# Kernel tuning notes

Measured on AMD Instinct MI355X. Metric: run time of the kernel, lower is better.

Reference implementation:

```python
import jax, jax.numpy as jnp
import numpy as np

N = 50000      # total nodes (batched graphs)
E = 800000     # edges per hop-set
B = 128        # number of graphs in batch
F_IN = 1024    # num_features_pro
D = 128        # hidden*16, heads=1


def setup_inputs() -> dict:
    key = jax.random.key(0)
    ks = jax.random.split(key, 32)
    s = 0.05
    def ei(k):
        return jax.random.randint(k, (2, E), 0, N, dtype=jnp.int32)
    inp = {
        'pro1_x': jax.random.normal(ks[0], (N, F_IN), jnp.float32),
        'pro1_ei1': ei(ks[1]), 'pro1_ei2': ei(ks[2]), 'pro1_ei3': ei(ks[3]),
        'pro1_batch': jnp.sort(jax.random.randint(ks[4], (N,), 0, B, dtype=jnp.int32)),
        'pro2_x': jax.random.normal(ks[5], (N, F_IN), jnp.float32),
        'pro2_ei1': ei(ks[6]), 'pro2_ei2': ei(ks[7]), 'pro2_ei3': ei(ks[8]),
        'pro2_batch': jnp.sort(jax.random.randint(ks[9], (N,), 0, B, dtype=jnp.int32)),
        # GATConv params (pro1_conv1 / pro2_conv1), shared across hop sets per branch
        'W1': jax.random.normal(ks[10], (F_IN, D), jnp.float32) * s,
        'a1_src': jax.random.normal(ks[11], (D,), jnp.float32) * s,
        'a1_dst': jax.random.normal(ks[12], (D,), jnp.float32) * s,
        'b1': jnp.zeros((D,), jnp.float32),
        'p1fc_W': jax.random.normal(ks[13], (D, D), jnp.float32) * s,
        'p1fc_b': jnp.zeros((D,), jnp.float32),
        'W2': jax.random.normal(ks[14], (F_IN, D), jnp.float32) * s,
        'a2_src': jax.random.normal(ks[15], (D,), jnp.float32) * s,
        'a2_dst': jax.random.normal(ks[16], (D,), jnp.float32) * s,
        'b2': jnp.zeros((D,), jnp.float32),
        'p2fc_W': jax.random.normal(ks[17], (D, D), jnp.float32) * s,
        'p2fc_b': jnp.zeros((D,), jnp.float32),
        'fc1_W': jax.random.normal(ks[18], (2 * D, 256), jnp.float32) * s,
        'fc1_b': jnp.zeros((256,), jnp.float32),
        'fc2_W': jax.random.normal(ks[19], (256, 64), jnp.float32) * s,
        'fc2_b': jnp.zeros((64,), jnp.float32),
        'out_W': jax.random.normal(ks[20], (64, 1), jnp.float32) * s,
        'out_b': jnp.zeros((1,), jnp.float32),
    }
    return inp


def _gat(x, ei, W, a_src, a_dst, b):
    # PyG GATConv, heads=1, add_self_loops=True, dropout off (eval)
    n = x.shape[0]
    h = x @ W                                   # [N, D]
    loops = jnp.arange(n, dtype=ei.dtype)
    src = jnp.concatenate([ei[0], loops])
    dst = jnp.concatenate([ei[1], loops])
    al_s = h @ a_src                            # [N]
    al_d = h @ a_dst
    e = jax.nn.leaky_relu(al_s[src] + al_d[dst], 0.2)   # per-edge logits
    m = jax.ops.segment_max(e, dst, num_segments=n)
    ex = jnp.exp(e - m[dst])
    denom = jax.ops.segment_sum(ex, dst, num_segments=n)
    alpha = ex / denom[dst]
    out = jax.ops.segment_sum(alpha[:, None] * h[src], dst, num_segments=n)
    return out + b


def _lrelu(v):
    return jax.nn.leaky_relu(v, 0.01)  # nn.LeakyReLU default slope


def _branch(x, e1, e2, e3, batch, W, a_s, a_d, b, fcW, fcb):
    h = _lrelu(_gat(x, e1, W, a_s, a_d, b))
    h = h + _lrelu(_gat(x, e2, W, a_s, a_d, b))
    h = h + _lrelu(_gat(x, e3, W, a_s, a_d, b))  # num_hops>=2 branch taken
    counts = jax.ops.segment_sum(jnp.ones((x.shape[0],), x.dtype), batch, num_segments=B)
    pooled = jax.ops.segment_sum(h, batch, num_segments=B) / jnp.maximum(counts, 1.0)[:, None]
    return _lrelu(pooled @ fcW + fcb)


def reference(pro1_x, pro1_ei1, pro1_ei2, pro1_ei3, pro1_batch,
              pro2_x, pro2_ei1, pro2_ei2, pro2_ei3, pro2_batch,
              W1, a1_src, a1_dst, b1, p1fc_W, p1fc_b,
              W2, a2_src, a2_dst, b2, p2fc_W, p2fc_b,
              fc1_W, fc1_b, fc2_W, fc2_b, out_W, out_b):
    x1 = _branch(pro1_x, pro1_ei1, pro1_ei2, pro1_ei3, pro1_batch, W1, a1_src, a1_dst, b1, p1fc_W, p1fc_b)
    x2 = _branch(pro2_x, pro2_ei1, pro2_ei2, pro2_ei3, pro2_batch, W2, a2_src, a2_dst, b2, p2fc_W, p2fc_b)
    xc = jnp.concatenate([x1, x2], axis=1)      # [B, 256]
    xc = _lrelu(xc @ fc1_W + fc1_b)
    xc = _lrelu(xc @ fc2_W + fc2_b)
    return jax.nn.sigmoid(xc @ out_W + out_b)   # [B, 1]
```

## Files before the change

kernel.cpp:

```cpp
#include <hip/hip_runtime.h>
#include <hip/hip_bf16.h>
#include <math.h>

#define N_NODES 50000
#define N_EDGES 800000
#define N_GRAPH 128
#define F_IN    1024
#define D_HID   128
#define NT3     (3*N_NODES)
#define LOG2E   1.44269504f

#define NPB_SH  9
#define NPB     512
#define NB      ((NT3 + NPB - 1) / NPB)
#define CAP     10240
#define EPB     4096
#define NBIN_PB ((3*N_EDGES + EPB - 1) / EPB)

typedef __bf16 bf16x8 __attribute__((ext_vector_type(8)));
typedef float  f32x4  __attribute__((ext_vector_type(4)));
typedef float  f32x2  __attribute__((ext_vector_type(2)));

__device__ __forceinline__ float lrelu01(float x){ return x > 0.f ? x : 0.01f*x; }
__device__ __forceinline__ float lrelu02(float x){ return x > 0.f ? x : 0.2f*x; }
__device__ __forceinline__ ushort f2bf(float v){
    __hip_bfloat16 hb = __float2bfloat16(v);
    return *reinterpret_cast<ushort*>(&hb);
}
__device__ __forceinline__ unsigned char f2fp8(float v){
    return (unsigned char)(__builtin_amdgcn_cvt_pk_fp8_f32(v, v, 0, false) & 0xFF);
}
__device__ __forceinline__ void fma8f8(uint2 u, float w, float* acc){
    f32x2 a = __builtin_amdgcn_cvt_pk_f32_fp8(u.x, false);
    f32x2 b = __builtin_amdgcn_cvt_pk_f32_fp8(u.x, true);
    f32x2 c = __builtin_amdgcn_cvt_pk_f32_fp8(u.y, false);
    f32x2 d = __builtin_amdgcn_cvt_pk_f32_fp8(u.y, true);
    acc[0] += w*a[0]; acc[1] += w*a[1]; acc[2] += w*b[0]; acc[3] += w*b[1];
    acc[4] += w*c[0]; acc[5] += w*c[1]; acc[6] += w*d[0]; acc[7] += w*d[1];
}

__global__ void k_prep(const float* __restrict__ W0, const float* __restrict__ W1,
                       ushort* __restrict__ Wt, int* __restrict__ gcur){
    int b = blockIdx.x, t = threadIdx.x;
    if (b < 1024){
        int idx = b*256 + t;
        int br  = idx >> 17;
        int r   = idx & 131071;
        int n = r >> 10, k = r & 1023;
        const float* W = br ? W1 : W0;
        Wt[idx] = f2bf(W[k*D_HID + n]);
    } else {
        for (int i=t; i<2*NB; i+=256) gcur[i] = 0;
    }
}

#define BM  64
#define BK  64
#define LDP 72

__global__ __launch_bounds__(256) void k_gemm(const float* __restrict__ X0, const float* __restrict__ X1,
                                              const ushort* __restrict__ Wt,
                                              const float* __restrict__ as0, const float* __restrict__ ad0,
                                              const float* __restrict__ as1, const float* __restrict__ ad1,
                                              unsigned char* __restrict__ H8,
                                              float* __restrict__ als, float* __restrict__ ald){
    __shared__ ushort As[BM*LDP];
    __shared__ ushort Bs[D_HID*LDP];
    __shared__ float alp[4][2][64];
    int br = blockIdx.y;
    const float*  X   = br ? X1 : X0;
    const float*  asr = br ? as1 : as0;
    const float*  adr = br ? ad1 : ad0;
    const ushort* Wtb = Wt + (size_t)br*D_HID*F_IN;
    unsigned char* Hbb = H8 + (size_t)br*N_NODES*D_HID;

    int tid  = threadIdx.x;
    int m0   = blockIdx.x * BM;
    int lane = tid & 63;
    int wave = tid >> 6;
    int l15 = lane & 15, l4 = lane >> 4;
    int wcol = wave * 32;

    float4 pa[4];
    uint4  pb[4];

    auto loadA = [&](int kt){
        #pragma unroll
        for (int i=0;i<4;i++){
            int q = tid + i*256; int row = q >> 4; int kq = (q & 15) << 2;
            int gr = m0 + row;
            pa[i] = (gr < N_NODES) ? *reinterpret_cast<const float4*>(X + (size_t)gr*F_IN + kt + kq)
                                   : make_float4(0.f,0.f,0.f,0.f);
        }
    };
    auto loadB = [&](int kt){
        #pragma unroll
        for (int i=0;i<4;i++){
            int q = tid + i*256; int row = q >> 3; int ck = q & 7;
            pb[i] = *reinterpret_cast<const uint4*>(Wtb + row*F_IN + kt + ck*8);
        }
    };
    auto stage = [&](){
        #pragma unroll
        for (int i=0;i<4;i++){
            int q = tid + i*256; int row = q >> 4; int kq = (q & 15) << 2;
            ushort4 b; b.x=f2bf(pa[i].x); b.y=f2bf(pa[i].y); b.z=f2bf(pa[i].z); b.w=f2bf(pa[i].w);
            *reinterpret_cast<ushort4*>(&As[row*LDP + kq]) = b;
        }
        #pragma unroll
        for (int i=0;i<4;i++){
            int q = tid + i*256; int row = q >> 3; int ck = q & 7;
            *reinterpret_cast<uint2*>(&Bs[row*LDP + ck*8])     = make_uint2(pb[i].x, pb[i].y);
            *reinterpret_cast<uint2*>(&Bs[row*LDP + ck*8 + 4]) = make_uint2(pb[i].z, pb[i].w);
        }
    };

    f32x4 acc[4][2];
    #pragma unroll
    for (int i=0;i<4;i++) for (int j=0;j<2;j++) acc[i][j] = (f32x4){0.f,0.f,0.f,0.f};

    loadA(0); loadB(0);
    for (int kt = 0; kt < F_IN; kt += BK) {
        stage();
        __syncthreads();
        if (kt + BK < F_IN){ loadA(kt+BK); loadB(kt+BK); }
        #pragma unroll
        for (int kk = 0; kk < BK; kk += 32) {
            bf16x8 af[4], bfr[2];
            #pragma unroll
            for (int mi=0;mi<4;mi++)
                af[mi] = *reinterpret_cast<const bf16x8*>(&As[(mi*16+l15)*LDP + kk + l4*8]);
            #pragma unroll
            for (int ni=0;ni<2;ni++)
                bfr[ni] = *reinterpret_cast<const bf16x8*>(&Bs[(wcol+ni*16+l15)*LDP + kk + l4*8]);
            #pragma unroll
            for (int mi=0;mi<4;mi++)
                #pragma unroll
                for (int ni=0;ni<2;ni++)
                    acc[mi][ni] = __builtin_amdgcn_mfma_f32_16x16x32_bf16(af[mi], bfr[ni], acc[mi][ni], 0,0,0);
        }
        __syncthreads();
    }

    float asv[2], adv[2];
    #pragma unroll
    for (int ni=0;ni<2;ni++){
        int c = wcol + ni*16 + l15;
        asv[ni] = asr[c]; adv[ni] = adr[c];
    }
    #pragma unroll
    for (int mi=0;mi<4;mi++){
        #pragma unroll
        for (int jj=0;jj<4;jj++){
            int rrel = mi*16 + l4*4 + jj;
            int r = m0 + rrel;
            float ps = 0.f, pd = 0.f;
            #pragma unroll
            for (int ni=0;ni<2;ni++){
                float v = acc[mi][ni][jj];
                ps += v*asv[ni]; pd += v*adv[ni];
                if (r < N_NODES){
                    int c = wcol + ni*16 + l15;
                    Hbb[(size_t)r*D_HID + c] = f2fp8(v);
                }
            }
            #pragma unroll
            for (int o=1;o<16;o<<=1){ ps += __shfl_xor(ps,o); pd += __shfl_xor(pd,o); }
            if (l15 == 0){ alp[wave][0][rrel] = ps; alp[wave][1][rrel] = pd; }
        }
    }
    __syncthreads();
    if (tid < 64){
        int r = m0 + tid;
        if (r < N_NODES){
            float s_ = alp[0][0][tid]+alp[1][0][tid]+alp[2][0][tid]+alp[3][0][tid];
            float d_ = alp[0][1][tid]+alp[1][1][tid]+alp[2][1][tid]+alp[3][1][tid];
            als[br*N_NODES + r] = s_;
            ald[br*N_NODES + r] = d_;
        }
    }
}

__global__ __launch_bounds__(256) void k_bin(const int* __restrict__ e10, const int* __restrict__ e20,
                                             const int* __restrict__ e30,
                                             const int* __restrict__ e11, const int* __restrict__ e21,
                                             const int* __restrict__ e31,
                                             int* __restrict__ gcur, uint* __restrict__ pairs){
    __shared__ int hist[NB];
    __shared__ int start[NB];
    int blk = blockIdx.x;
    int br    = blk / NBIN_PB;
    int chunk = blk - br*NBIN_PB;
    int tid = threadIdx.x;
    for (int b=tid; b<NB; b+=256) hist[b]=0;
    __syncthreads();
    long base = (long)chunk * EPB;
    int  myb[16]; uint mypk[16];
    #pragma unroll
    for (int i=0;i<16;i++){
        long idx = base + i*256 + tid;
        int b = -1; uint pk = 0;
        if (idx < 3L*N_EDGES){
            int hop = (idx >= 2L*N_EDGES) ? 2 : (idx >= (long)N_EDGES) ? 1 : 0;
            int e   = (int)(idx - (long)hop*N_EDGES);
            const int* ei = (br==0) ? ((hop==0)?e10:(hop==1)?e20:e30)
                                    : ((hop==0)?e11:(hop==1)?e21:e31);
            int src = ei[e];
            int vd  = hop*N_NODES + ei[N_EDGES + e];
            b   = vd >> NPB_SH;
            pk  = (uint)src | ((uint)(vd & (NPB-1)) << 16);
            atomicAdd(&hist[b], 1);
        }
        myb[i]=b; mypk[i]=pk;
    }
    __syncthreads();
    for (int b=tid; b<NB; b+=256){
        int h = hist[b];
        start[b] = (h>0) ? atomicAdd(&gcur[br*NB + b], h) : 0;
    }
    __syncthreads();
    for (int b=tid; b<NB; b+=256) hist[b] = start[b];
    __syncthreads();
    #pragma unroll
    for (int i=0;i<16;i++){
        int b = myb[i];
        if (b >= 0){
            int pos = atomicAdd(&hist[b], 1);
            if (pos < CAP) pairs[((size_t)(br*NB + b))*CAP + pos] = mypk[i];
        }
    }
}

__global__ __launch_bounds__(256) void k_localcsr(const int* __restrict__ gcur,
                                                  const uint* __restrict__ pairs,
                                                  int* __restrict__ offs3, int* __restrict__ esrc){
    __shared__ int sc[512];
    __shared__ int deg[NPB];
    __shared__ int cur[NPB];
    __shared__ int ss[256];
    int gb = blockIdx.x;
    int br = gb / NB, bb = gb - br*NB;
    int t = threadIdx.x;
    sc[t]     = (t < NB)       ? min(gcur[br*NB + t], CAP) : 0;
    sc[t+256] = (t+256 < NB)   ? min(gcur[br*NB + t+256], CAP) : 0;
    __syncthreads();
    for (int o=1;o<512;o<<=1){
        int v0 = (t>=o)     ? sc[t-o]     : 0;
        int v1 = (t+256>=o) ? sc[t+256-o] : 0;
        __syncthreads();
        sc[t] += v0; sc[t+256] += v1;
        __syncthreads();
    }
    int base = (bb==0) ? 0 : sc[bb-1];
    int cnt  = sc[bb] - base;
    int* offsb = offs3 + (size_t)br*(NT3+1);
    if (bb == NB-1 && t == 0) offsb[NT3] = sc[NB-1];

    deg[t]=0; deg[t+256]=0;
    __syncthreads();
    const uint* pbuf = pairs + ((size_t)(br*NB + bb))*CAP;
    for (int i=t; i<cnt; i+=256) atomicAdd(&deg[pbuf[i] >> 16], 1);
    __syncthreads();
    int a0 = deg[2*t], a1 = deg[2*t+1];
    int ps = a0 + a1;
    ss[t] = ps; __syncthreads();
    for (int o=1;o<256;o<<=1){
        int u = (t>=o) ? ss[t-o] : 0;
        __syncthreads(); ss[t] += u; __syncthreads();
    }
    int ex = ss[t] - ps;
    __syncthreads();
    deg[2*t] = ex; deg[2*t+1] = ex + a0;
    cur[2*t] = ex; cur[2*t+1] = ex + a0;
    __syncthreads();
    int vd0 = bb << NPB_SH;
    for (int l=t; l<NPB; l+=256){
        int vd = vd0 + l;
        if (vd < NT3) offsb[vd] = base + deg[l];
    }
    int* esrcb = esrc + (size_t)br*3*N_EDGES;
    for (int i=t; i<cnt; i+=256){
        uint p = pbuf[i];
        int pos = atomicAdd(&cur[p >> 16], 1);
        esrcb[base + pos] = (int)(p & 0xFFFFu);
    }
}

__global__ __launch_bounds__(256) void k_gat3(const int* __restrict__ offs3, const int* __restrict__ esrc3,
                     const float* __restrict__ als, const float* __restrict__ ald,
                     const uint2* __restrict__ H8,
                     const float* __restrict__ bv0, const float* __restrict__ bv1,
                     float* __restrict__ hacc){
    __shared__ uint2 sh[4][64];
    int br = blockIdx.y;
    const int*   offs = offs3 + (size_t)br*(NT3+1);
    const int*   esrc = esrc3 + (size_t)br*3*N_EDGES;
    const float* alsb = als + br*N_NODES;
    const float* aldb = ald + br*N_NODES;
    const uint2* H8b  = H8 + (size_t)br*N_NODES*16;
    const float* bvec = br ? bv1 : bv0;
    float*       hb   = hacc + (size_t)br*N_NODES*D_HID;

    int lane = threadIdx.x & 63;
    int wl   = threadIdx.x >> 6;
    int d = blockIdx.x*4 + wl;
    if (d >= N_NODES) return;
    int g  = lane >> 4;
    int fl = lane & 15;
    float aldd  = aldb[d];
    float eself = lrelu02(alsb[d] + aldd);
    float exs   = __builtin_amdgcn_exp2f(eself * LOG2E);
    uint2 hs = H8b[(size_t)d*16 + fl];
    float hself[8];
    { f32x2 a = __builtin_amdgcn_cvt_pk_f32_fp8(hs.x, false);
      f32x2 b = __builtin_amdgcn_cvt_pk_f32_fp8(hs.x, true);
      f32x2 c = __builtin_amdgcn_cvt_pk_f32_fp8(hs.y, false);
      f32x2 d2 = __builtin_amdgcn_cvt_pk_f32_fp8(hs.y, true);
      hself[0]=a[0];hself[1]=a[1];hself[2]=b[0];hself[3]=b[1];
      hself[4]=c[0];hself[5]=c[1];hself[6]=d2[0];hself[7]=d2[1]; }
    float bvv[8];
    #pragma unroll
    for (int k=0;k<8;k++) bvv[k] = bvec[fl*8+k];
    float tot[8] = {0.f,0.f,0.f,0.f,0.f,0.f,0.f,0.f};

    for (int hop=0; hop<3; hop++){
        int s0 = offs[hop*N_NODES + d];
        int s1 = offs[hop*N_NODES + d + 1];
        int deg = s1 - s0;
        float acc[8];
        #pragma unroll
        for (int k=0;k<8;k++) acc[k] = (g==0) ? exs*hself[k] : 0.f;
        float es = 0.f;
        for (int base=0; base<deg; base+=64){
            int j = base + lane;
            int s = 0; float ex = 0.f;
            if (j < deg){
                s = esrc[s0 + j];
                ex = __builtin_amdgcn_exp2f(lrelu02(alsb[s] + aldd) * LOG2E);
            }
            es += ex;
            sh[wl][lane] = make_uint2((uint)s, __float_as_uint(ex));
            int cnt = min(64, deg - base);
            int i = g;
            for (; i + 4 < cnt; i += 8){
                uint2 seA = sh[wl][i];
                uint2 seB = sh[wl][i+4];
                uint2 hvA = H8b[(size_t)seA.x*16 + fl];
                uint2 hvB = H8b[(size_t)seB.x*16 + fl];
                fma8f8(hvA, __uint_as_float(seA.y), acc);
                fma8f8(hvB, __uint_as_float(seB.y), acc);
            }
            if (i < cnt){
                uint2 se = sh[wl][i];
                uint2 hv = H8b[(size_t)se.x*16 + fl];
                fma8f8(hv, __uint_as_float(se.y), acc);
            }
        }
        for (int o=32;o;o>>=1) es += __shfl_xor(es,o);
        #pragma unroll
        for (int k=0;k<8;k++){
            acc[k] += __shfl_xor(acc[k], 16);
            acc[k] += __shfl_xor(acc[k], 32);
        }
        float inv = 1.f / (es + exs);
        #pragma unroll
        for (int k=0;k<8;k++) tot[k] += lrelu01(acc[k]*inv + bvv[k]);
    }
    if (g == 0){
        float4 w0 = make_float4(tot[0],tot[1],tot[2],tot[3]);
        float4 w1 = make_float4(tot[4],tot[5],tot[6],tot[7]);
        *reinterpret_cast<float4*>(hb + (size_t)d*D_HID + fl*8)     = w0;
        *reinterpret_cast<float4*>(hb + (size_t)d*D_HID + fl*8 + 4) = w1;
    }
}

__global__ __launch_bounds__(256) void k_pool_fc(const float* __restrict__ hacc,
                    const int* __restrict__ b0, const int* __restrict__ b1,
                    const float* __restrict__ pW0, const float* __restrict__ pb0,
                    const float* __restrict__ pW1, const float* __restrict__ pb1,
                    float* __restrict__ xb){
    __shared__ float sums[2][128];
    __shared__ float pl[128];
    int br = blockIdx.y;
    const float* hb   = hacc + (size_t)br*N_NODES*D_HID;
    const int*   batch= br ? b1 : b0;
    const float* fcW  = br ? pW1 : pW0;
    const float* fcb  = br ? pb1 : pb0;
    int g = blockIdx.x;
    int t = threadIdx.x;
    int lo=0, hi=N_NODES;
    while (lo<hi){ int mid=(lo+hi)>>1; if (batch[mid] < g) lo=mid+1; else hi=mid; }
    int s = lo;
    lo = s; hi = N_NODES;
    while (lo<hi){ int mid=(lo+hi)>>1; if (batch[mid] < g+1) lo=mid+1; else hi=mid; }
    int e = lo;
    int f = t & 127, half = t >> 7;
    float sum = 0.f;
    for (int n=s+half; n<e; n+=2) sum += hb[(size_t)n*D_HID + f];
    sums[half][f] = sum;
    __syncthreads();
    if (t < 128){
        float cnt = (float)(e - s);
        pl[t] = (sums[0][t] + sums[1][t]) / fmaxf(cnt, 1.0f);
    }
    __syncthreads();
    if (t < 128){
        float a = fcb[t];
        for (int k=0;k<128;k++) a += pl[k]*fcW[k*128 + t];
        xb[(br*N_GRAPH + g)*128 + t] = lrelu01(a);
    }
}

__global__ __launch_bounds__(256) void k_final(const float* __restrict__ xb,
                      const float* __restrict__ fc1W, const float* __restrict__ fc1b,
                      const float* __restrict__ fc2W, const float* __restrict__ fc2b,
                      const float* __restrict__ outW, const float* __restrict__ outb,
                      float* __restrict__ out){
    __shared__ float xc[256], y1[256], y2[64];
    int g = blockIdx.x, t = threadIdx.x;
    xc[t] = (t < 128) ? xb[g*128 + t] : xb[(N_GRAPH + g)*128 + (t-128)];
    __syncthreads();
    float a = fc1b[t];
    for (int k=0;k<256;k++) a += xc[k]*fc1W[k*256 + t];
    y1[t] = lrelu01(a);
    __syncthreads();
    if (t < 64){
        float a2 = fc2b[t];
        for (int k=0;k<256;k++) a2 += y1[k]*fc2W[k*64 + t];
        y2[t] = lrelu01(a2);
    }
    __syncthreads();
    if (t == 0){
        float z = outb[0];
        for (int k=0;k<64;k++) z += y2[k]*outW[k];
        out[g] = 1.f/(1.f + expf(-z));
    }
}

extern "C" void kernel_launch(void* const* d_in, const int* in_sizes, int n_in,
                              void* d_out, int out_size, void* d_ws, size_t ws_size,
                              hipStream_t stream){
    const float* X0 = (const float*)d_in[0];
    const float* X1 = (const float*)d_in[5];
    const int *e10=(const int*)d_in[1], *e20=(const int*)d_in[2], *e30=(const int*)d_in[3];
    const int *e11=(const int*)d_in[6], *e21=(const int*)d_in[7], *e31=(const int*)d_in[8];
    const int *b0=(const int*)d_in[4], *b1=(const int*)d_in[9];
    const float *W0=(const float*)d_in[10], *W1=(const float*)d_in[16];
    const float *as0=(const float*)d_in[11], *ad0=(const float*)d_in[12];
    const float *as1=(const float*)d_in[17], *ad1=(const float*)d_in[18];
    const float *bv0=(const float*)d_in[13], *bv1=(const float*)d_in[19];
    const float *pW0=(const float*)d_in[14], *pb0=(const float*)d_in[15];
    const float *pW1=(const float*)d_in[20], *pb1=(const float*)d_in[21];
    const float *fc1W=(const float*)d_in[22], *fc1b=(const float*)d_in[23];
    const float *fc2W=(const float*)d_in[24], *fc2b=(const float*)d_in[25];
    const float *outW=(const float*)d_in[26], *outb=(const float*)d_in[27];
    float* out = (float*)d_out;

    char* ws = (char*)d_ws;
    size_t o = 0;
    auto alloc = [&](size_t bytes)->char*{ char* p = ws + o; o += (bytes + 511) & ~(size_t)511; return p; };
    unsigned char* H8 = (unsigned char*)alloc((size_t)2*N_NODES*D_HID);
    float*  hacc  = (float*) alloc((size_t)2*N_NODES*D_HID*4);
    float*  als   = (float*) alloc((size_t)2*N_NODES*4);
    float*  ald   = (float*) alloc((size_t)2*N_NODES*4);
    int*    offs3 = (int*)   alloc((size_t)2*(NT3+1)*4);
    int*    esrc3 = (int*)   alloc((size_t)2*3*N_EDGES*4);
    int*    gcur  = (int*)   alloc((size_t)2*NB*4);
    uint*   pairs = (uint*)  alloc((size_t)2*NB*CAP*4);
    ushort* Wt    = (ushort*)alloc((size_t)2*D_HID*F_IN*2);
    float*  xb    = (float*) alloc((size_t)2*N_GRAPH*D_HID*4);

    k_prep    <<<1025, 256, 0, stream>>>(W0, W1, Wt, gcur);
    k_gemm    <<<dim3((N_NODES+BM-1)/BM, 2), 256, 0, stream>>>(X0, X1, Wt, as0, ad0, as1, ad1, H8, als, ald);
    k_bin     <<<2*NBIN_PB, 256, 0, stream>>>(e10, e20, e30, e11, e21, e31, gcur, pairs);
    k_localcsr<<<2*NB, 256, 0, stream>>>(gcur, pairs, offs3, esrc3);
    k_gat3    <<<dim3((N_NODES+3)/4, 2), 256, 0, stream>>>(offs3, esrc3, als, ald, (const uint2*)H8, bv0, bv1, hacc);
    k_pool_fc <<<dim3(N_GRAPH, 2), 256, 0, stream>>>(hacc, b0, b1, pW0, pb0, pW1, pb1, xb);
    k_final   <<<N_GRAPH, 256, 0, stream>>>(xb, fc1W, fc1b, fc2W, fc2b, outW, outb, out);
}
```

Measured before the change: 424.4 us.

## Pack source attention logit with edge source index and use packed FP32 FMAs

The CSR build now stores each edge as a (source, als[source]) pair, so the aggregation kernel no longer does a dependent random gather of als per edge. The gather moves into k_localcsr, and the edge array doubles in size, adding write and read traffic. Separately, the fp8 feature accumulation is rewritten with 2-wide float vectors so the compiler can emit packed FMA instructions.

```diff
diff --git a/kernel.cpp b/kernel.cpp
--- a/kernel.cpp
+++ b/kernel.cpp
@@ -30,13 +30,11 @@
 __device__ __forceinline__ unsigned char f2fp8(float v){
     return (unsigned char)(__builtin_amdgcn_cvt_pk_fp8_f32(v, v, 0, false) & 0xFF);
 }
-__device__ __forceinline__ void fma8f8(uint2 u, float w, float* acc){
-    f32x2 a = __builtin_amdgcn_cvt_pk_f32_fp8(u.x, false);
-    f32x2 b = __builtin_amdgcn_cvt_pk_f32_fp8(u.x, true);
-    f32x2 c = __builtin_amdgcn_cvt_pk_f32_fp8(u.y, false);
-    f32x2 d = __builtin_amdgcn_cvt_pk_f32_fp8(u.y, true);
-    acc[0] += w*a[0]; acc[1] += w*a[1]; acc[2] += w*b[0]; acc[3] += w*b[1];
-    acc[4] += w*c[0]; acc[5] += w*c[1]; acc[6] += w*d[0]; acc[7] += w*d[1];
+__device__ __forceinline__ void fma8pk(uint2 u, f32x2 w2, f32x2* acc2){
+    acc2[0] += w2 * __builtin_amdgcn_cvt_pk_f32_fp8(u.x, false);
+    acc2[1] += w2 * __builtin_amdgcn_cvt_pk_f32_fp8(u.x, true);
+    acc2[2] += w2 * __builtin_amdgcn_cvt_pk_f32_fp8(u.y, false);
+    acc2[3] += w2 * __builtin_amdgcn_cvt_pk_f32_fp8(u.y, true);
 }
 
 __global__ void k_prep(const float* __restrict__ W0, const float* __restrict__ W1,
@@ -233,7 +231,8 @@
 
 __global__ __launch_bounds__(256) void k_localcsr(const int* __restrict__ gcur,
                                                   const uint* __restrict__ pairs,
-                                                  int* __restrict__ offs3, int* __restrict__ esrc){
+                                                  const float* __restrict__ als,
+                                                  int* __restrict__ offs3, uint2* __restrict__ esrc){
     __shared__ int sc[512];
     __shared__ int deg[NPB];
     __shared__ int cur[NPB];
@@ -278,15 +277,18 @@
         int vd = vd0 + l;
         if (vd < NT3) offsb[vd] = base + deg[l];
     }
-    int* esrcb = esrc + (size_t)br*3*N_EDGES;
+    const float* alsb = als + br*N_NODES;
+    uint2* esrcb = esrc + (size_t)br*3*N_EDGES;
     for (int i=t; i<cnt; i+=256){
         uint p = pbuf[i];
+        uint src = p & 0xFFFFu;
+        float av = alsb[src];
         int pos = atomicAdd(&cur[p >> 16], 1);
-        esrcb[base + pos] = (int)(p & 0xFFFFu);
-    }
-}
-
-__global__ __launch_bounds__(256) void k_gat3(const int* __restrict__ offs3, const int* __restrict__ esrc3,
+        esrcb[base + pos] = make_uint2(src, __float_as_uint(av));
+    }
+}
+
+__global__ __launch_bounds__(256) void k_gat3(const int* __restrict__ offs3, const uint2* __restrict__ esrc3,
                      const float* __restrict__ als, const float* __restrict__ ald,
                      const uint2* __restrict__ H8,
                      const float* __restrict__ bv0, const float* __restrict__ bv1,
@@ -294,7 +296,7 @@
     __shared__ uint2 sh[4][64];
     int br = blockIdx.y;
     const int*   offs = offs3 + (size_t)br*(NT3+1);
-    const int*   esrc = esrc3 + (size_t)br*3*N_EDGES;
+    const uint2* esrc = esrc3 + (size_t)br*3*N_EDGES;
     const float* alsb = als + br*N_NODES;
     const float* aldb = ald + br*N_NODES;
     const uint2* H8b  = H8 + (size_t)br*N_NODES*16;
@@ -310,33 +312,37 @@
     float aldd  = aldb[d];
     float eself = lrelu02(alsb[d] + aldd);
     float exs   = __builtin_amdgcn_exp2f(eself * LOG2E);
-    uint2 hs = H8b[(size_t)d*16 + fl];
-    float hself[8];
-    { f32x2 a = __builtin_amdgcn_cvt_pk_f32_fp8(hs.x, false);
-      f32x2 b = __builtin_amdgcn_cvt_pk_f32_fp8(hs.x, true);
-      f32x2 c = __builtin_amdgcn_cvt_pk_f32_fp8(hs.y, false);
-      f32x2 d2 = __builtin_amdgcn_cvt_pk_f32_fp8(hs.y, true);
-      hself[0]=a[0];hself[1]=a[1];hself[2]=b[0];hself[3]=b[1];
-      hself[4]=c[0];hself[5]=c[1];hself[6]=d2[0];hself[7]=d2[1]; }
-    float bvv[8];
-    #pragma unroll
-    for (int k=0;k<8;k++) bvv[k] = bvec[fl*8+k];
-    float tot[8] = {0.f,0.f,0.f,0.f,0.f,0.f,0.f,0.f};
+    f32x2 self2[4];
+    {
+        uint2 hs = H8b[(size_t)d*16 + fl];
+        f32x2 w2 = (f32x2){exs, exs};
+        self2[0] = w2 * __builtin_amdgcn_cvt_pk_f32_fp8(hs.x, false);
+        self2[1] = w2 * __builtin_amdgcn_cvt_pk_f32_fp8(hs.x, true);
+        self2[2] = w2 * __builtin_amdgcn_cvt_pk_f32_fp8(hs.y, false);
+        self2[3] = w2 * __builtin_amdgcn_cvt_pk_f32_fp8(hs.y, true);
+    }
+    f32x2 bv2[4];
+    #pragma unroll
+    for (int k=0;k<4;k++) bv2[k] = (f32x2){bvec[fl*8+2*k], bvec[fl*8+2*k+1]};
+    f32x2 tot2[4];
+    #pragma unroll
+    for (int k=0;k<4;k++) tot2[k] = (f32x2){0.f, 0.f};
 
     for (int hop=0; hop<3; hop++){
         int s0 = offs[hop*N_NODES + d];
         int s1 = offs[hop*N_NODES + d + 1];
         int deg = s1 - s0;
-        float acc[8];
-        #pragma unroll
-        for (int k=0;k<8;k++) acc[k] = (g==0) ? exs*hself[k] : 0.f;
+        f32x2 acc2[4];
+        #pragma unroll
+        for (int k=0;k<4;k++) acc2[k] = (g==0) ? self2[k] : (f32x2){0.f,0.f};
         float es = 0.f;
         for (int base=0; base<deg; base+=64){
             int j = base + lane;
             int s = 0; float ex = 0.f;
             if (j < deg){
-                s = esrc[s0 + j];
-                ex = __builtin_amdgcn_exp2f(lrelu02(alsb[s] + aldd) * LOG2E);
+                uint2 ev = esrc[s0 + j];
+                s = (int)ev.x;
+                ex = __builtin_amdgcn_exp2f(lrelu02(__uint_as_float(ev.y) + aldd) * LOG2E);
             }
             es += ex;
             sh[wl][lane] = make_uint2((uint)s, __float_as_uint(ex));
@@ -347,28 +353,36 @@
                 uint2 seB = sh[wl][i+4];
                 uint2 hvA = H8b[(size_t)seA.x*16 + fl];
                 uint2 hvB = H8b[(size_t)seB.x*16 + fl];
-                fma8f8(hvA, __uint_as_float(seA.y), acc);
-                fma8f8(hvB, __uint_as_float(seB.y), acc);
+                float wA = __uint_as_float(seA.y);
+                float wB = __uint_as_float(seB.y);
+                fma8pk(hvA, (f32x2){wA,wA}, acc2);
+                fma8pk(hvB, (f32x2){wB,wB}, acc2);
             }
             if (i < cnt){
                 uint2 se = sh[wl][i];
                 uint2 hv = H8b[(size_t)se.x*16 + fl];
-                fma8f8(hv, __uint_as_float(se.y), acc);
+                float w = __uint_as_float(se.y);
+                fma8pk(hv, (f32x2){w,w}, acc2);
             }
         }
         for (int o=32;o;o>>=1) es += __shfl_xor(es,o);
         #pragma unroll
-        for (int k=0;k<8;k++){
-            acc[k] += __shfl_xor(acc[k], 16);
-            acc[k] += __shfl_xor(acc[k], 32);
+        for (int k=0;k<4;k++){
+            float x0 = acc2[k][0], x1 = acc2[k][1];
+            x0 += __shfl_xor(x0, 16); x0 += __shfl_xor(x0, 32);
+            x1 += __shfl_xor(x1, 16); x1 += __shfl_xor(x1, 32);
+            acc2[k][0] = x0; acc2[k][1] = x1;
         }
         float inv = 1.f / (es + exs);
         #pragma unroll
-        for (int k=0;k<8;k++) tot[k] += lrelu01(acc[k]*inv + bvv[k]);
+        for (int k=0;k<4;k++){
+            tot2[k][0] += lrelu01(acc2[k][0]*inv + bv2[k][0]);
+            tot2[k][1] += lrelu01(acc2[k][1]*inv + bv2[k][1]);
+        }
     }
     if (g == 0){
-        float4 w0 = make_float4(tot[0],tot[1],tot[2],tot[3]);
-        float4 w1 = make_float4(tot[4],tot[5],tot[6],tot[7]);
+        float4 w0 = make_float4(tot2[0][0],tot2[0][1],tot2[1][0],tot2[1][1]);
+        float4 w1 = make_float4(tot2[2][0],tot2[2][1],tot2[3][0],tot2[3][1]);
         *reinterpret_cast<float4*>(hb + (size_t)d*D_HID + fl*8)     = w0;
         *reinterpret_cast<float4*>(hb + (size_t)d*D_HID + fl*8 + 4) = w1;
     }
@@ -464,7 +478,7 @@
     float*  als   = (float*) alloc((size_t)2*N_NODES*4);
     float*  ald   = (float*) alloc((size_t)2*N_NODES*4);
     int*    offs3 = (int*)   alloc((size_t)2*(NT3+1)*4);
-    int*    esrc3 = (int*)   alloc((size_t)2*3*N_EDGES*4);
+    uint2*  esrc3 = (uint2*) alloc((size_t)2*3*N_EDGES*8);
     int*    gcur  = (int*)   alloc((size_t)2*NB*4);
     uint*   pairs = (uint*)  alloc((size_t)2*NB*CAP*4);
     ushort* Wt    = (ushort*)alloc((size_t)2*D_HID*F_IN*2);
@@ -473,7 +487,7 @@
     k_prep    <<<1025, 256, 0, stream>>>(W0, W1, Wt, gcur);
     k_gemm    <<<dim3((N_NODES+BM-1)/BM, 2), 256, 0, stream>>>(X0, X1, Wt, as0, ad0, as1, ad1, H8, als, ald);
     k_bin     <<<2*NBIN_PB, 256, 0, stream>>>(e10, e20, e30, e11, e21, e31, gcur, pairs);
-    k_localcsr<<<2*NB, 256, 0, stream>>>(gcur, pairs, offs3, esrc3);
+    k_localcsr<<<2*NB, 256, 0, stream>>>(gcur, pairs, als, offs3, esrc3);
     k_gat3    <<<dim3((N_NODES+3)/4, 2), 256, 0, stream>>>(offs3, esrc3, als, ald, (const uint2*)H8, bv0, bv1, hacc);
     k_pool_fc <<<dim3(N_GRAPH, 2), 256, 0, stream>>>(hacc, b0, b1, pW0, pb0, pW1, pb1, xb);
     k_final   <<<N_GRAPH, 256, 0, stream>>>(xb, fc1W, fc1b, fc2W, fc2b, outW, outb, out);
```

Result: slower. 445.5 us (+5.0%).

## Split GAT aggregation into feature halves with interleaved block mapping

Applied to the files above, without the earlier changes.

The GAT aggregation kernel now gives each block only half of the 128 fp8 features (64 bytes per row), with a 1D grid whose block index is decoded into branch, feature half and node group. Adjacent blocks share the same node and branch but cover different feature halves, so gathered rows may be reused in L2. Each thread now handles 4 features instead of 8, which lowers register pressure and doubles the block count. The cost is that edge indices, attention exps and softmax sums are recomputed once per half, and each gather is a narrower 4-byte load per lane.

```diff
diff --git a/kernel.cpp b/kernel.cpp
--- a/kernel.cpp
+++ b/kernel.cpp
@@ -30,13 +30,10 @@
 __device__ __forceinline__ unsigned char f2fp8(float v){
     return (unsigned char)(__builtin_amdgcn_cvt_pk_fp8_f32(v, v, 0, false) & 0xFF);
 }
-__device__ __forceinline__ void fma8f8(uint2 u, float w, float* acc){
-    f32x2 a = __builtin_amdgcn_cvt_pk_f32_fp8(u.x, false);
-    f32x2 b = __builtin_amdgcn_cvt_pk_f32_fp8(u.x, true);
-    f32x2 c = __builtin_amdgcn_cvt_pk_f32_fp8(u.y, false);
-    f32x2 d = __builtin_amdgcn_cvt_pk_f32_fp8(u.y, true);
+__device__ __forceinline__ void fma4f8(uint u, float w, float* acc){
+    f32x2 a = __builtin_amdgcn_cvt_pk_f32_fp8(u, false);
+    f32x2 b = __builtin_amdgcn_cvt_pk_f32_fp8(u, true);
     acc[0] += w*a[0]; acc[1] += w*a[1]; acc[2] += w*b[0]; acc[3] += w*b[1];
-    acc[4] += w*c[0]; acc[5] += w*c[1]; acc[6] += w*d[0]; acc[7] += w*d[1];
 }
 
 __global__ void k_prep(const float* __restrict__ W0, const float* __restrict__ W1,
@@ -288,48 +285,51 @@
 
 __global__ __launch_bounds__(256) void k_gat3(const int* __restrict__ offs3, const int* __restrict__ esrc3,
                      const float* __restrict__ als, const float* __restrict__ ald,
-                     const uint2* __restrict__ H8,
+                     const uint* __restrict__ H8u,
                      const float* __restrict__ bv0, const float* __restrict__ bv1,
                      float* __restrict__ hacc){
     __shared__ uint2 sh[4][64];
-    int br = blockIdx.y;
+    int bid   = blockIdx.x;
+    int combo = (bid & 7) >> 1;
+    int br    = combo >> 1;
+    int fh    = combo & 1;
+    int sub   = ((bid >> 3) << 1) | (bid & 1);
+
     const int*   offs = offs3 + (size_t)br*(NT3+1);
     const int*   esrc = esrc3 + (size_t)br*3*N_EDGES;
     const float* alsb = als + br*N_NODES;
     const float* aldb = ald + br*N_NODES;
-    const uint2* H8b  = H8 + (size_t)br*N_NODES*16;
+    const uint*  Hrow = H8u + (size_t)br*N_NODES*32 + fh*16;
     const float* bvec = br ? bv1 : bv0;
     float*       hb   = hacc + (size_t)br*N_NODES*D_HID;
 
     int lane = threadIdx.x & 63;
     int wl   = threadIdx.x >> 6;
-    int d = blockIdx.x*4 + wl;
+    int d = sub*4 + wl;
     if (d >= N_NODES) return;
     int g  = lane >> 4;
     int fl = lane & 15;
     float aldd  = aldb[d];
     float eself = lrelu02(alsb[d] + aldd);
     float exs   = __builtin_amdgcn_exp2f(eself * LOG2E);
-    uint2 hs = H8b[(size_t)d*16 + fl];
-    float hself[8];
-    { f32x2 a = __builtin_amdgcn_cvt_pk_f32_fp8(hs.x, false);
-      f32x2 b = __builtin_amdgcn_cvt_pk_f32_fp8(hs.x, true);
-      f32x2 c = __builtin_amdgcn_cvt_pk_f32_fp8(hs.y, false);
-      f32x2 d2 = __builtin_amdgcn_cvt_pk_f32_fp8(hs.y, true);
-      hself[0]=a[0];hself[1]=a[1];hself[2]=b[0];hself[3]=b[1];
-      hself[4]=c[0];hself[5]=c[1];hself[6]=d2[0];hself[7]=d2[1]; }
-    float bvv[8];
-    #pragma unroll
-    for (int k=0;k<8;k++) bvv[k] = bvec[fl*8+k];
-    float tot[8] = {0.f,0.f,0.f,0.f,0.f,0.f,0.f,0.f};
+    float hself[4];
+    {
+        uint hs = Hrow[(size_t)d*32 + fl];
+        hself[0]=0.f; hself[1]=0.f; hself[2]=0.f; hself[3]=0.f;
+        fma4f8(hs, 1.f, hself);
+    }
+    float bvv[4];
+    #pragma unroll
+    for (int k=0;k<4;k++) bvv[k] = bvec[fh*64 + fl*4 + k];
+    float tot[4] = {0.f,0.f,0.f,0.f};
 
     for (int hop=0; hop<3; hop++){
         int s0 = offs[hop*N_NODES + d];
         int s1 = offs[hop*N_NODES + d + 1];
         int deg = s1 - s0;
-        float acc[8];
-        #pragma unroll
-        for (int k=0;k<8;k++) acc[k] = (g==0) ? exs*hself[k] : 0.f;
+        float acc[4];
+        #pragma unroll
+        for (int k=0;k<4;k++) acc[k] = (g==0) ? exs*hself[k] : 0.f;
         float es = 0.f;
         for (int base=0; base<deg; base+=64){
             int j = base + lane;
@@ -345,32 +345,30 @@
             for (; i + 4 < cnt; i += 8){
                 uint2 seA = sh[wl][i];
                 uint2 seB = sh[wl][i+4];
-                uint2 hvA = H8b[(size_t)seA.x*16 + fl];
-                uint2 hvB = H8b[(size_t)seB.x*16 + fl];
-                fma8f8(hvA, __uint_as_float(seA.y), acc);
-                fma8f8(hvB, __uint_as_float(seB.y), acc);
+                uint hvA = Hrow[(size_t)seA.x*32 + fl];
+                uint hvB = Hrow[(size_t)seB.x*32 + fl];
+                fma4f8(hvA, __uint_as_float(seA.y), acc);
+                fma4f8(hvB, __uint_as_float(seB.y), acc);
             }
             if (i < cnt){
                 uint2 se = sh[wl][i];
-                uint2 hv = H8b[(size_t)se.x*16 + fl];
-                fma8f8(hv, __uint_as_float(se.y), acc);
+                uint hv = Hrow[(size_t)se.x*32 + fl];
+                fma4f8(hv, __uint_as_float(se.y), acc);
             }
         }
         for (int o=32;o;o>>=1) es += __shfl_xor(es,o);
         #pragma unroll
-        for (int k=0;k<8;k++){
+        for (int k=0;k<4;k++){
             acc[k] += __shfl_xor(acc[k], 16);
             acc[k] += __shfl_xor(acc[k], 32);
         }
         float inv = 1.f / (es + exs);
         #pragma unroll
-        for (int k=0;k<8;k++) tot[k] += lrelu01(acc[k]*inv + bvv[k]);
+        for (int k=0;k<4;k++) tot[k] += lrelu01(acc[k]*inv + bvv[k]);
     }
     if (g == 0){
-        float4 w0 = make_float4(tot[0],tot[1],tot[2],tot[3]);
-        float4 w1 = make_float4(tot[4],tot[5],tot[6],tot[7]);
-        *reinterpret_cast<float4*>(hb + (size_t)d*D_HID + fl*8)     = w0;
-        *reinterpret_cast<float4*>(hb + (size_t)d*D_HID + fl*8 + 4) = w1;
+        float4 w = make_float4(tot[0],tot[1],tot[2],tot[3]);
+        *reinterpret_cast<float4*>(hb + (size_t)d*D_HID + fh*64 + fl*4) = w;
     }
 }
 
@@ -474,7 +472,7 @@
     k_gemm    <<<dim3((N_NODES+BM-1)/BM, 2), 256, 0, stream>>>(X0, X1, Wt, as0, ad0, as1, ad1, H8, als, ald);
     k_bin     <<<2*NBIN_PB, 256, 0, stream>>>(e10, e20, e30, e11, e21, e31, gcur, pairs);
     k_localcsr<<<2*NB, 256, 0, stream>>>(gcur, pairs, offs3, esrc3);
-    k_gat3    <<<dim3((N_NODES+3)/4, 2), 256, 0, stream>>>(offs3, esrc3, als, ald, (const uint2*)H8, bv0, bv1, hacc);
+    k_gat3    <<<N_NODES, 256, 0, stream>>>(offs3, esrc3, als, ald, (const uint*)H8, bv0, bv1, hacc);
     k_pool_fc <<<dim3(N_GRAPH, 2), 256, 0, stream>>>(hacc, b0, b1, pW0, pb0, pW1, pb1, xb);
     k_final   <<<N_GRAPH, 256, 0, stream>>>(xb, fc1W, fc1b, fc2W, fc2b, outW, outb, out);
 }
```

Result: slower. 483.1 us (+13.8%).
